# Performance work log

Hardware: AMD Instinct MI355X
Metric: run time of the kernel (lower is better)

## Reference

```python
import jax, jax.numpy as jnp
import numpy as np

N_NODES = 100000
N_EDGES = 3200000


def gcn_conv(x, W, b, src, dst, n_nodes):
    """PyG GCNConv: self-loops, symmetric D^-1/2 A D^-1/2 norm, linear, bias."""
    loop = jnp.arange(n_nodes, dtype=src.dtype)
    s = jnp.concatenate([src, loop])  # [E+N]
    d = jnp.concatenate([dst, loop])  # [E+N]
    # degree computed at destination (col), edge_weight = 1
    deg = jax.ops.segment_sum(jnp.ones_like(d, dtype=x.dtype), d,
                              num_segments=n_nodes)
    dinv = jnp.where(deg > 0, jax.lax.rsqrt(deg), 0.0)
    norm = dinv[s] * dinv[d]  # [E+N]
    h = x @ W.T  # [N, out]
    msg = h[s] * norm[:, None]  # gather + scale, [E+N, out]
    out = jax.ops.segment_sum(msg, d, num_segments=n_nodes)  # scatter-add
    return out + b


def setup_inputs() -> dict:
    key = jax.random.key(0)
    k1, k2, k3, k4 = jax.random.split(key, 4)
    x = jax.random.normal(k1, (N_NODES, 2), dtype=jnp.float32)
    edge_index = jax.random.randint(k2, (2, N_EDGES), 0, N_NODES,
                                    dtype=jnp.int64)
    # Glorot-ish init for linear weights
    W1 = jax.random.normal(k3, (64, 2), dtype=jnp.float32) * 0.5
    b1 = jnp.zeros((64,), dtype=jnp.float32)
    W2 = jax.random.normal(k4, (2, 64), dtype=jnp.float32) * 0.125
    b2 = jnp.zeros((2,), dtype=jnp.float32)
    return {"x": x, "edge_index": edge_index, "W1": W1, "b1": b1,
            "W2": W2, "b2": b2}


def reference(x, edge_index, W1, b1, W2, b2):
    src, dst = edge_index[0], edge_index[1]
    h = gcn_conv(x, W1, b1, src, dst, N_NODES)
    h = jax.nn.relu(h)
    out = gcn_conv(h, W2, b2, src, dst, N_NODES)
    return out
```

## Files before the change

kernel.cpp:

```cpp
#include <hip/hip_runtime.h>

#define N_NODES 100000
#define SHIFT 9
#define BNODES 512
#define NB 196
#define CAP 18432
#define TILE 8192
#define SB 512


__global__ __launch_bounds__(SB) void k_sort(const int* __restrict__ src,
                                             const int* __restrict__ dst,
                                             int* claim, int* sg, int e) {
    __shared__ int hist[NB];
    __shared__ int scanb[256];
    __shared__ int start[NB];
    __shared__ int runbase[NB];
    __shared__ int stage[TILE];
    __shared__ unsigned char binmap[TILE];

    const int t = threadIdx.x;
    const int base = blockIdx.x * TILE;
    const int n = min(TILE, e - base);

    for (int i = t; i < NB; i += SB) hist[i] = 0;
    __syncthreads();

    int recs[16];
    int bins[16];
#pragma unroll
    for (int k = 0; k < 4; ++k) {
        int idx = base + (k * SB + t) * 4;
        if (idx + 3 < e) {
            int4 s4 = *(const int4*)(src + idx);
            int4 d4 = *(const int4*)(dst + idx);
            int ss[4] = {s4.x, s4.y, s4.z, s4.w};
            int dd[4] = {d4.x, d4.y, d4.z, d4.w};
#pragma unroll
            for (int j = 0; j < 4; ++j) {
                int b = dd[j] >> SHIFT;
                bins[4 * k + j] = b;
                recs[4 * k + j] = ss[j] | ((dd[j] & (BNODES - 1)) << 17);
                atomicAdd(&hist[b], 1);
            }
        } else {
#pragma unroll
            for (int j = 0; j < 4; ++j) {
                int i2 = idx + j;
                if (i2 < e) {
                    int d = dst[i2];
                    int b = d >> SHIFT;
                    bins[4 * k + j] = b;
                    recs[4 * k + j] = src[i2] | ((d & (BNODES - 1)) << 17);
                    atomicAdd(&hist[b], 1);
                } else {
                    bins[4 * k + j] = -1;
                }
            }
        }
    }
    __syncthreads();

    if (t < 256) scanb[t] = (t < NB) ? hist[t] : 0;
    __syncthreads();
    for (int off = 1; off < 256; off <<= 1) {
        int w = (t < 256 && t >= off) ? scanb[t - off] : 0;
        __syncthreads();
        if (t < 256) scanb[t] += w;
        __syncthreads();
    }
    if (t < NB) {
        int c = hist[t];
        int excl = scanb[t] - c;
        start[t] = excl;
        scanb[t] = excl;
        runbase[t] = c ? atomicAdd(&claim[t], c) : 0;
    }
    __syncthreads();

#pragma unroll
    for (int m = 0; m < 16; ++m) {
        int b = bins[m];
        if (b >= 0) {
            int pos = atomicAdd(&scanb[b], 1);
            stage[pos] = recs[m];
            binmap[pos] = (unsigned char)b;
        }
    }
    __syncthreads();

    for (int i = t; i < n; i += SB) {
        int b = binmap[i];
        sg[b * CAP + runbase[b] + (i - start[b])] = stage[i];
    }
}

__global__ __launch_bounds__(1024) void k_refine(const int* __restrict__ claim,
                                                 const int* __restrict__ sg,
                                                 const float* __restrict__ x,
                                                 int* sg2, int* packed,
                                                 float2* u) {
    __shared__ int hist[BNODES];
    __shared__ int scanb[BNODES];
    const int t = threadIdx.x;
    const int b = blockIdx.x;
    const int* p = sg + b * CAP;
    const int len = claim[b];

    int4 r[5];
#pragma unroll
    for (int k = 0; k < 5; ++k) {
        int idx = 4 * t + 4096 * k;
        int4 v = make_int4(-1, -1, -1, -1);
        if (idx + 3 < len) v = *(const int4*)(p + idx);
        else if (idx < len) {
            v.x = p[idx];
            if (idx + 1 < len) v.y = p[idx + 1];
            if (idx + 2 < len) v.z = p[idx + 2];
        }
        r[k] = v;
    }
    if (t < BNODES) hist[t] = 0;
    __syncthreads();
#pragma unroll
    for (int k = 0; k < 5; ++k) {
        if (r[k].x != -1) atomicAdd(&hist[((unsigned)r[k].x) >> 17], 1);
        if (r[k].y != -1) atomicAdd(&hist[((unsigned)r[k].y) >> 17], 1);
        if (r[k].z != -1) atomicAdd(&hist[((unsigned)r[k].z) >> 17], 1);
        if (r[k].w != -1) atomicAdd(&hist[((unsigned)r[k].w) >> 17], 1);
    }
    __syncthreads();

    if (t < BNODES) scanb[t] = hist[t];
    __syncthreads();
    for (int off = 1; off < BNODES; off <<= 1) {
        int w = (t >= off && t < BNODES) ? scanb[t - off] : 0;
        __syncthreads();
        if (t < BNODES) scanb[t] += w;
        __syncthreads();
    }
    if (t < BNODES) {
        int mycnt = hist[t];
        int myexcl = scanb[t] - mycnt;
        int node = b * BNODES + t;
        if (node < N_NODES) {
            packed[node] = (b * CAP + myexcl) | (mycnt << 22);
            float dv = rsqrtf((float)(mycnt + 1));
            float2 xv = ((const float2*)x)[node];
            u[node] = make_float2(dv * xv.x, dv * xv.y);
        }
        hist[t] = myexcl;
    }
    __syncthreads();

    int* q = sg2 + b * CAP;
#pragma unroll
    for (int k = 0; k < 5; ++k) {
        if (r[k].x != -1) q[atomicAdd(&hist[((unsigned)r[k].x) >> 17], 1)] = r[k].x & 0x1FFFF;
        if (r[k].y != -1) q[atomicAdd(&hist[((unsigned)r[k].y) >> 17], 1)] = r[k].y & 0x1FFFF;
        if (r[k].z != -1) q[atomicAdd(&hist[((unsigned)r[k].z) >> 17], 1)] = r[k].z & 0x1FFFF;
        if (r[k].w != -1) q[atomicAdd(&hist[((unsigned)r[k].w) >> 17], 1)] = r[k].w & 0x1FFFF;
    }
}

__global__ __launch_bounds__(256) void k_agg1(const int* __restrict__ sg2,
                                              const int* __restrict__ packed,
                                              const float2* __restrict__ u,
                                              const float* __restrict__ W1,
                                              const float* __restrict__ b1,
                                              const float* __restrict__ W2,
                                              float2* v) {
    __shared__ float sW1[128], sb1[64], sW2[128];
    int t = threadIdx.x;
    if (t < 128) { sW1[t] = W1[t]; sW2[t] = W2[t]; }
    else if (t < 192) sb1[t - 128] = b1[t - 128];
    __syncthreads();
    int n = blockIdx.x * 32 + (t >> 3);
    if (n >= N_NODES) return;
    int g = t & 7;
    int pk = packed[n];
    int s = pk & 0x3FFFFF;
    int cnt = ((unsigned)pk) >> 22;
    int e2 = s + cnt;
    float sx = 0.f, sy = 0.f;
    int i = s + g;
    for (; i + 8 < e2; i += 16) {
        float2 ga = u[sg2[i]];
        float2 gb = u[sg2[i + 8]];
        sx += ga.x + gb.x;
        sy += ga.y + gb.y;
    }
    if (i < e2) { float2 ga = u[sg2[i]]; sx += ga.x; sy += ga.y; }
    sx += __shfl_xor(sx, 1, 8); sy += __shfl_xor(sy, 1, 8);
    sx += __shfl_xor(sx, 2, 8); sy += __shfl_xor(sy, 2, 8);
    sx += __shfl_xor(sx, 4, 8); sy += __shfl_xor(sy, 4, 8);
    float dv = rsqrtf((float)(cnt + 1));
    float2 un = u[n];
    float a0 = dv * (sx + un.x), a1 = dv * (sy + un.y);
    float y0 = 0.f, y1 = 0.f;
#pragma unroll
    for (int k = 0; k < 8; ++k) {
        int j = g + 8 * k;
        float h = fmaxf(fmaf(sW1[2 * j], a0,
                        fmaf(sW1[2 * j + 1], a1, sb1[j])), 0.f);
        y0 = fmaf(sW2[j], h, y0);
        y1 = fmaf(sW2[64 + j], h, y1);
    }
    y0 += __shfl_xor(y0, 1, 8); y1 += __shfl_xor(y1, 1, 8);
    y0 += __shfl_xor(y0, 2, 8); y1 += __shfl_xor(y1, 2, 8);
    y0 += __shfl_xor(y0, 4, 8); y1 += __shfl_xor(y1, 4, 8);
    if (g == 0) v[n] = make_float2(dv * y0, dv * y1);
}

__global__ __launch_bounds__(256) void k_agg2(const int* __restrict__ sg2,
                                              const int* __restrict__ packed,
                                              const float2* __restrict__ v,
                                              const float* __restrict__ b2,
                                              float2* out) {
    int t = threadIdx.x;
    int n = blockIdx.x * 32 + (t >> 3);
    if (n >= N_NODES) return;
    int g = t & 7;
    int pk = packed[n];
    int s = pk & 0x3FFFFF;
    int cnt = ((unsigned)pk) >> 22;
    int e2 = s + cnt;
    float sx = 0.f, sy = 0.f;
    int i = s + g;
    for (; i + 8 < e2; i += 16) {
        float2 ga = v[sg2[i]];
        float2 gb = v[sg2[i + 8]];
        sx += ga.x + gb.x;
        sy += ga.y + gb.y;
    }
    if (i < e2) { float2 ga = v[sg2[i]]; sx += ga.x; sy += ga.y; }
    sx += __shfl_xor(sx, 1, 8); sy += __shfl_xor(sy, 1, 8);
    sx += __shfl_xor(sx, 2, 8); sy += __shfl_xor(sy, 2, 8);
    sx += __shfl_xor(sx, 4, 8); sy += __shfl_xor(sy, 4, 8);
    if (g == 0) {
        float dv = rsqrtf((float)(cnt + 1));
        float2 vn = v[n];
        out[n] = make_float2(fmaf(dv, sx + vn.x, b2[0]),
                             fmaf(dv, sy + vn.y, b2[1]));
    }
}

extern "C" void kernel_launch(void* const* d_in, const int* in_sizes, int n_in,
                              void* d_out, int out_size, void* d_ws, size_t ws_size,
                              hipStream_t stream) {
    const float* x  = (const float*)d_in[0];
    const int* ei   = (const int*)d_in[1];
    const float* W1 = (const float*)d_in[2];
    const float* b1 = (const float*)d_in[3];
    const float* W2 = (const float*)d_in[4];
    const float* b2 = (const float*)d_in[5];

    int e = in_sizes[1] / 2;
    const int* src = ei;
    const int* dst = ei + e;

    int* ws      = (int*)d_ws;
    int* claim   = ws;
    int* sg      = ws + NB;
    int* sg2     = sg + NB * CAP;
    int* packed  = sg2 + NB * CAP;
    float2* u    = (float2*)(packed + N_NODES);
    float2* v    = u + N_NODES;
    float2* outp = (float2*)d_out;

    hipMemsetAsync(claim, 0, NB * sizeof(int), stream);

    const int gA = (N_NODES + 31) / 32;
    k_sort  <<<(e + TILE - 1) / TILE, SB, 0, stream>>>(src, dst, claim, sg, e);
    k_refine<<<NB, 1024, 0, stream>>>(claim, sg, x, sg2, packed, u);
    k_agg1  <<<gA, 256, 0, stream>>>(sg2, packed, u, W1, b1, W2, v);
    k_agg2  <<<gA, 256, 0, stream>>>(sg2, packed, v, b2, outp);
}
```

Before: 153.7 us.

## Halve bucket size, privatize shared histograms, use wave-shuffle scans, unroll gathers

Coarse buckets shrink from 512 to 256 nodes (391 buckets, smaller capacity), so the refine pass holds 3 int4 per thread instead of 5. The sort and refine kernels now keep 2 and 4 private LDS histogram copies per thread group to cut atomic contention, and replace the barrier-heavy Hillis-Steele scans with wavefront shuffle scans. The sort scatter precomputes one address base per bin. The aggregation loops are unrolled to 4 independent gathers per iteration for more memory-level parallelism. The costs are more LDS per block, a 16-bit bin map, and more global claim atomics with smaller per-bin runs.

```diff
diff --git a/kernel.cpp b/kernel.cpp
--- a/kernel.cpp
+++ b/kernel.cpp
@@ -1,10 +1,10 @@
 #include <hip/hip_runtime.h>
 
 #define N_NODES 100000
-#define SHIFT 9
-#define BNODES 512
-#define NB 196
-#define CAP 18432
+#define SHIFT 8
+#define BNODES 256
+#define NB 391
+#define CAP 9728
 #define TILE 8192
 #define SB 512
 
@@ -12,22 +12,24 @@
 __global__ __launch_bounds__(SB) void k_sort(const int* __restrict__ src,
                                              const int* __restrict__ dst,
                                              int* claim, int* sg, int e) {
-    __shared__ int hist[NB];
-    __shared__ int scanb[256];
-    __shared__ int start[NB];
-    __shared__ int runbase[NB];
+    __shared__ int hist[2 * NB];
+    __shared__ int rank[2 * NB];
+    __shared__ int addrbase[NB];
+    __shared__ int partials[8];
     __shared__ int stage[TILE];
-    __shared__ unsigned char binmap[TILE];
+    __shared__ unsigned short binmap[TILE];
 
     const int t = threadIdx.x;
     const int base = blockIdx.x * TILE;
     const int n = min(TILE, e - base);
-
-    for (int i = t; i < NB; i += SB) hist[i] = 0;
+    const int goff = (t >> 8) * NB;
+
+    for (int i = t; i < 2 * NB; i += SB) hist[i] = 0;
     __syncthreads();
 
     int recs[16];
     int bins[16];
+    int* myh = hist + goff;
 #pragma unroll
     for (int k = 0; k < 4; ++k) {
         int idx = base + (k * SB + t) * 4;
@@ -41,7 +43,7 @@
                 int b = dd[j] >> SHIFT;
                 bins[4 * k + j] = b;
                 recs[4 * k + j] = ss[j] | ((dd[j] & (BNODES - 1)) << 17);
-                atomicAdd(&hist[b], 1);
+                atomicAdd(&myh[b], 1);
             }
         } else {
 #pragma unroll
@@ -52,7 +54,7 @@
                     int b = d >> SHIFT;
                     bins[4 * k + j] = b;
                     recs[4 * k + j] = src[i2] | ((d & (BNODES - 1)) << 17);
-                    atomicAdd(&hist[b], 1);
+                    atomicAdd(&myh[b], 1);
                 } else {
                     bins[4 * k + j] = -1;
                 }
@@ -61,20 +63,25 @@
     }
     __syncthreads();
 
-    if (t < 256) scanb[t] = (t < NB) ? hist[t] : 0;
-    __syncthreads();
-    for (int off = 1; off < 256; off <<= 1) {
-        int w = (t < 256 && t >= off) ? scanb[t - off] : 0;
-        __syncthreads();
-        if (t < 256) scanb[t] += w;
-        __syncthreads();
-    }
+    int c0 = (t < NB) ? hist[t] : 0;
+    int c = c0 + ((t < NB) ? hist[NB + t] : 0);
+    int vs = c;
+#pragma unroll
+    for (int off = 1; off < 64; off <<= 1) {
+        int w = __shfl_up(vs, off, 64);
+        if ((t & 63) >= off) vs += w;
+    }
+    if ((t & 63) == 63) partials[t >> 6] = vs;
+    __syncthreads();
+    int add = 0;
+    for (int w = 0; w < (t >> 6); ++w) add += partials[w];
+    vs += add;
+    int excl = vs - c;
     if (t < NB) {
-        int c = hist[t];
-        int excl = scanb[t] - c;
-        start[t] = excl;
-        scanb[t] = excl;
-        runbase[t] = c ? atomicAdd(&claim[t], c) : 0;
+        rank[t] = excl;
+        rank[NB + t] = excl + c0;
+        int rb = c ? atomicAdd(&claim[t], c) : 0;
+        addrbase[t] = t * CAP + rb - excl;
     }
     __syncthreads();
 
@@ -82,16 +89,15 @@
     for (int m = 0; m < 16; ++m) {
         int b = bins[m];
         if (b >= 0) {
-            int pos = atomicAdd(&scanb[b], 1);
+            int pos = atomicAdd(&rank[goff + b], 1);
             stage[pos] = recs[m];
-            binmap[pos] = (unsigned char)b;
+            binmap[pos] = (unsigned short)b;
         }
     }
     __syncthreads();
 
     for (int i = t; i < n; i += SB) {
-        int b = binmap[i];
-        sg[b * CAP + runbase[b] + (i - start[b])] = stage[i];
+        sg[addrbase[binmap[i]] + i] = stage[i];
     }
 }
 
@@ -100,16 +106,18 @@
                                                  const float* __restrict__ x,
                                                  int* sg2, int* packed,
                                                  float2* u) {
-    __shared__ int hist[BNODES];
-    __shared__ int scanb[BNODES];
+    __shared__ int hist[4 * BNODES];
+    __shared__ int rank[4 * BNODES];
+    __shared__ int partials[4];
     const int t = threadIdx.x;
     const int b = blockIdx.x;
     const int* p = sg + b * CAP;
     const int len = claim[b];
-
-    int4 r[5];
-#pragma unroll
-    for (int k = 0; k < 5; ++k) {
+    const int g = t >> 8;
+
+    int4 r[3];
+#pragma unroll
+    for (int k = 0; k < 3; ++k) {
         int idx = 4 * t + 4096 * k;
         int4 v = make_int4(-1, -1, -1, -1);
         if (idx + 3 < len) v = *(const int4*)(p + idx);
@@ -120,46 +128,62 @@
         }
         r[k] = v;
     }
-    if (t < BNODES) hist[t] = 0;
-    __syncthreads();
-#pragma unroll
-    for (int k = 0; k < 5; ++k) {
-        if (r[k].x != -1) atomicAdd(&hist[((unsigned)r[k].x) >> 17], 1);
-        if (r[k].y != -1) atomicAdd(&hist[((unsigned)r[k].y) >> 17], 1);
-        if (r[k].z != -1) atomicAdd(&hist[((unsigned)r[k].z) >> 17], 1);
-        if (r[k].w != -1) atomicAdd(&hist[((unsigned)r[k].w) >> 17], 1);
-    }
-    __syncthreads();
-
-    if (t < BNODES) scanb[t] = hist[t];
-    __syncthreads();
-    for (int off = 1; off < BNODES; off <<= 1) {
-        int w = (t >= off && t < BNODES) ? scanb[t - off] : 0;
-        __syncthreads();
-        if (t < BNODES) scanb[t] += w;
-        __syncthreads();
-    }
+    for (int i = t; i < 4 * BNODES; i += 1024) hist[i] = 0;
+    __syncthreads();
+    int* myh = hist + g * BNODES;
+#pragma unroll
+    for (int k = 0; k < 3; ++k) {
+        if (r[k].x != -1) atomicAdd(&myh[((unsigned)r[k].x) >> 17], 1);
+        if (r[k].y != -1) atomicAdd(&myh[((unsigned)r[k].y) >> 17], 1);
+        if (r[k].z != -1) atomicAdd(&myh[((unsigned)r[k].z) >> 17], 1);
+        if (r[k].w != -1) atomicAdd(&myh[((unsigned)r[k].w) >> 17], 1);
+    }
+    __syncthreads();
+
+    int c4x = 0, c4y = 0, c4z = 0, c4w = 0, tot = 0;
     if (t < BNODES) {
-        int mycnt = hist[t];
-        int myexcl = scanb[t] - mycnt;
+        c4x = hist[t];
+        c4y = hist[BNODES + t];
+        c4z = hist[2 * BNODES + t];
+        c4w = hist[3 * BNODES + t];
+        tot = (c4x + c4y) + (c4z + c4w);
+    }
+    int vs = tot;
+#pragma unroll
+    for (int off = 1; off < 64; off <<= 1) {
+        int w = __shfl_up(vs, off, 64);
+        if ((t & 63) >= off) vs += w;
+    }
+    if ((t & 63) == 63 && t < BNODES) partials[t >> 6] = vs;
+    __syncthreads();
+    if (t < BNODES) {
+        int add = 0;
+        for (int w = 0; w < (t >> 6); ++w) add += partials[w];
+        vs += add;
+        int excl = vs - tot;
+        int run = excl;
+        rank[t] = run; run += c4x;
+        rank[BNODES + t] = run; run += c4y;
+        rank[2 * BNODES + t] = run; run += c4z;
+        rank[3 * BNODES + t] = run;
         int node = b * BNODES + t;
         if (node < N_NODES) {
-            packed[node] = (b * CAP + myexcl) | (mycnt << 22);
-            float dv = rsqrtf((float)(mycnt + 1));
+            packed[node] = (b * CAP + excl) | (tot << 22);
+            float dv = rsqrtf((float)(tot + 1));
             float2 xv = ((const float2*)x)[node];
             u[node] = make_float2(dv * xv.x, dv * xv.y);
         }
-        hist[t] = myexcl;
     }
     __syncthreads();
 
     int* q = sg2 + b * CAP;
-#pragma unroll
-    for (int k = 0; k < 5; ++k) {
-        if (r[k].x != -1) q[atomicAdd(&hist[((unsigned)r[k].x) >> 17], 1)] = r[k].x & 0x1FFFF;
-        if (r[k].y != -1) q[atomicAdd(&hist[((unsigned)r[k].y) >> 17], 1)] = r[k].y & 0x1FFFF;
-        if (r[k].z != -1) q[atomicAdd(&hist[((unsigned)r[k].z) >> 17], 1)] = r[k].z & 0x1FFFF;
-        if (r[k].w != -1) q[atomicAdd(&hist[((unsigned)r[k].w) >> 17], 1)] = r[k].w & 0x1FFFF;
+    int* myr = rank + g * BNODES;
+#pragma unroll
+    for (int k = 0; k < 3; ++k) {
+        if (r[k].x != -1) q[atomicAdd(&myr[((unsigned)r[k].x) >> 17], 1)] = r[k].x & 0x1FFFF;
+        if (r[k].y != -1) q[atomicAdd(&myr[((unsigned)r[k].y) >> 17], 1)] = r[k].y & 0x1FFFF;
+        if (r[k].z != -1) q[atomicAdd(&myr[((unsigned)r[k].z) >> 17], 1)] = r[k].z & 0x1FFFF;
+        if (r[k].w != -1) q[atomicAdd(&myr[((unsigned)r[k].w) >> 17], 1)] = r[k].w & 0x1FFFF;
     }
 }
 
@@ -184,6 +208,14 @@
     int e2 = s + cnt;
     float sx = 0.f, sy = 0.f;
     int i = s + g;
+    for (; i + 24 < e2; i += 32) {
+        float2 ga = u[sg2[i]];
+        float2 gb = u[sg2[i + 8]];
+        float2 gc = u[sg2[i + 16]];
+        float2 gd = u[sg2[i + 24]];
+        sx += (ga.x + gb.x) + (gc.x + gd.x);
+        sy += (ga.y + gb.y) + (gc.y + gd.y);
+    }
     for (; i + 8 < e2; i += 16) {
         float2 ga = u[sg2[i]];
         float2 gb = u[sg2[i + 8]];
@@ -227,6 +259,14 @@
     int e2 = s + cnt;
     float sx = 0.f, sy = 0.f;
     int i = s + g;
+    for (; i + 24 < e2; i += 32) {
+        float2 ga = v[sg2[i]];
+        float2 gb = v[sg2[i + 8]];
+        float2 gc = v[sg2[i + 16]];
+        float2 gd = v[sg2[i + 24]];
+        sx += (ga.x + gb.x) + (gc.x + gd.x);
+        sy += (ga.y + gb.y) + (gc.y + gd.y);
+    }
     for (; i + 8 < e2; i += 16) {
         float2 ga = v[sg2[i]];
         float2 gb = v[sg2[i + 8]];
@@ -261,7 +301,7 @@
 
     int* ws      = (int*)d_ws;
     int* claim   = ws;
-    int* sg      = ws + NB;
+    int* sg      = ws + ((NB + 3) & ~3);
     int* sg2     = sg + NB * CAP;
     int* packed  = sg2 + NB * CAP;
     float2* u    = (float2*)(packed + N_NODES);
```

New measurement: 152.3 us. No clear change (-0.9%).
